# Kernel optimization log

Hardware: AMD Instinct MI355X
Metric: run time of the kernel (lower is better)

Reference implementation:

```python
import jax, jax.numpy as jnp
import numpy as np

N = 2048      # nodes (= in_features = out_features, forced by h0 @ adj)
C = 512       # channels
B = 8         # batch
NNZ = 65536   # number of edges (avg degree 32)
NEG = -9e15   # masked-fill value from the source


def setup_inputs() -> dict:
    key = jax.random.key(0)
    k1, k2, k3, k4 = jax.random.split(key, 4)
    x = jax.random.normal(k1, (B, C, N), dtype=jnp.float32)
    # xavier_normal_ with gain=0.01: std = gain * sqrt(2/(fan_in+fan_out))
    std = 0.01 * float(np.sqrt(2.0 / (N + N)))
    W1 = jax.random.normal(k2, (N, N), dtype=jnp.float32) * std
    W2 = jax.random.normal(k3, (N, N), dtype=jnp.float32) * std
    # e is initialized to 1 in the source; perturb so softmax is non-trivial
    e = 1.0 + 0.1 * jax.random.normal(k4, (NNZ,), dtype=jnp.float32)
    # flat row-major indices of mask nonzeros, unique + sorted (matches adj[mask] = e)
    rng = np.random.default_rng(0)
    edge_idx = np.sort(rng.choice(N * N, size=NNZ, replace=False)).astype(np.int64)
    return {"x": x, "W1": W1, "W2": W2, "e": e, "edge_idx": jnp.asarray(edge_idx)}


def reference(x, W1, W2, e, edge_idx):
    # h0, h1: [B, C, N]
    h0 = jnp.matmul(x, W1)
    h1 = jnp.matmul(x, W2)
    # scatter per-edge logits into dense [N, N], masked positions = -9e15
    logits = jnp.full((N * N,), NEG, dtype=jnp.float32).at[edge_idx].set(e)
    A = jax.nn.softmax(logits.reshape(N, N), axis=1)  # row-wise softmax
    diag = jnp.diagonal(A)                 # A * I  (self term, diagonal scaling)
    A_off = A - jnp.diag(diag)             # A * (1 - I)  (neighbor term)
    # h0 @ (A*I) == h0 scaled per-node by diag; h1 @ (A*(1-I)) dense GEMM
    out = h0 * diag[None, None, :] + jnp.matmul(h1, A_off)
    return out  # [B, C, N]; torch squeeze is a no-op here; bias=False
```

## Files before the change

### kernel.cpp

```cpp
#include <hip/hip_runtime.h>
#include <hip/hip_bf16.h>
#include <stdint.h>

#define NN 2048
#define LOG2NN 11
#define GK 2048
#define GNC 2048

typedef __bf16 bf16x8 __attribute__((ext_vector_type(8)));
typedef float f32x4 __attribute__((ext_vector_type(4)));

__device__ __forceinline__ ushort f2bf(float f) {
  uint32_t x = __float_as_uint(f);
  uint32_t r = (x + 0x7fffu + ((x >> 16) & 1u)) >> 16;
  return (ushort)r;
}

__global__ __launch_bounds__(256) void prep_kernel(
    const float* __restrict__ W1, const float* __restrict__ W2,
    ushort* __restrict__ WT, ushort* __restrict__ W2T,
    const float* __restrict__ x, ushort* __restrict__ xb,
    int* __restrict__ hist, float* __restrict__ uW, int* __restrict__ ecnt) {
  __shared__ float tile[64][65];
  const int bid = blockIdx.x;
  const int t = threadIdx.x;
  if (bid < 2048) {
    const int m = bid >> 10;
    const int rem = bid & 1023;
    const int r0 = (rem >> 5) * 64, c0 = (rem & 31) * 64;
    const float* in = m ? W2 : W1;
    ushort* out = m ? W2T : WT;
    const int tx = t & 15, ty = t >> 4;
#pragma unroll
    for (int i = 0; i < 4; ++i) {
      int r = i * 16 + ty;
      float4 v = *reinterpret_cast<const float4*>(&in[(size_t)(r0 + r) * NN + c0 + tx * 4]);
      tile[r][tx * 4 + 0] = v.x;
      tile[r][tx * 4 + 1] = v.y;
      tile[r][tx * 4 + 2] = v.z;
      tile[r][tx * 4 + 3] = v.w;
    }
    __syncthreads();
#pragma unroll
    for (int i = 0; i < 4; ++i) {
      int oc = i * 16 + ty;
      ushort4 o;
      o.x = f2bf(tile[tx * 4 + 0][oc]);
      o.y = f2bf(tile[tx * 4 + 1][oc]);
      o.z = f2bf(tile[tx * 4 + 2][oc]);
      o.w = f2bf(tile[tx * 4 + 3][oc]);
      *reinterpret_cast<ushort4*>(&out[(size_t)(c0 + oc) * NN + r0 + tx * 4]) = o;
    }
  } else if (bid < 6144) {
    int i = (bid - 2048) * 256 + t;
    const float4* in4 = reinterpret_cast<const float4*>(x);
    float4 a = in4[2 * i];
    float4 b = in4[2 * i + 1];
    uint4 o;
    o.x = (uint32_t)f2bf(a.x) | ((uint32_t)f2bf(a.y) << 16);
    o.y = (uint32_t)f2bf(a.z) | ((uint32_t)f2bf(a.w) << 16);
    o.z = (uint32_t)f2bf(b.x) | ((uint32_t)f2bf(b.y) << 16);
    o.w = (uint32_t)f2bf(b.z) | ((uint32_t)f2bf(b.w) << 16);
    reinterpret_cast<uint4*>(xb)[i] = o;
  } else {
#pragma unroll
    for (int j = 0; j < 8; ++j) {
      hist[t * 8 + j] = 0;
      uW[t * 8 + j] = 0.f;
    }
    if (t == 0) *ecnt = 0;
  }
}

__device__ __forceinline__ int lower_bound32(const int* __restrict__ a, int n, int v) {
  int lo = 0, hi = n;
  while (lo < hi) {
    int mid = (lo + hi) >> 1;
    if (a[mid] < v) lo = mid + 1; else hi = mid;
  }
  return lo;
}

__global__ __launch_bounds__(256) void softmax_hist_kernel(
    const int* __restrict__ idx, const float* __restrict__ e, int nnz,
    float* __restrict__ vals, float* __restrict__ diag, int* __restrict__ empty,
    int* __restrict__ ecnt, int* __restrict__ hist) {
  const int w = threadIdx.x >> 6, lane = threadIdx.x & 63;
  const int r = blockIdx.x * 4 + w;
  int lo = lower_bound32(idx, nnz, r << LOG2NN);
  int hi = lower_bound32(idx, nnz, (r + 1) << LOG2NN);
  if (hi <= lo) {
    if (lane == 0) { diag[r] = 1.0f / NN; empty[r] = 1; atomicAdd(ecnt, 1); }
    return;
  }
  float m = -3.0e38f;
  for (int j = lo + lane; j < hi; j += 64) m = fmaxf(m, e[j]);
#pragma unroll
  for (int s = 32; s >= 1; s >>= 1) m = fmaxf(m, __shfl_xor(m, s));
  float sum = 0.f;
  for (int j = lo + lane; j < hi; j += 64) sum += expf(e[j] - m);
#pragma unroll
  for (int s = 32; s >= 1; s >>= 1) sum += __shfl_xor(sum, s);
  float inv = 1.0f / sum;
  float dv = 0.f;
  for (int j = lo + lane; j < hi; j += 64) {
    float v = expf(e[j] - m) * inv;
    vals[j] = v;
    int c = idx[j] & (NN - 1);
    if (c == r) dv = v;
    else atomicAdd(&hist[c], 1);
  }
#pragma unroll
  for (int s = 32; s >= 1; s >>= 1) dv += __shfl_xor(dv, s);
  if (lane == 0) { diag[r] = dv; empty[r] = 0; }
}

__global__ __launch_bounds__(256) void scan_uw_kernel(
    const int* __restrict__ hist, int* __restrict__ base, int* __restrict__ cursor,
    const float* __restrict__ W2, const int* __restrict__ empty,
    const int* __restrict__ ecnt, float* __restrict__ uW) {
  if (blockIdx.x == 0) {
    const int l = threadIdx.x;
    if (l >= 64) return;
    int vals[32], pre[32];
    int run = 0;
#pragma unroll
    for (int j = 0; j < 32; ++j) {
      vals[j] = hist[l * 32 + j];
      pre[j] = run;
      run += vals[j];
    }
    int tot = run, inc = run;
#pragma unroll
    for (int s = 1; s < 64; s <<= 1) {
      int o = __shfl_up(inc, s);
      if (l >= s) inc += o;
    }
    int excl = inc - tot;
#pragma unroll
    for (int j = 0; j < 32; ++j) {
      int b = excl + pre[j];
      base[l * 32 + j] = b;
      cursor[l * 32 + j] = b;
    }
  } else {
    if (*ecnt == 0) return;
    int p = (blockIdx.x - 1) * 256 + threadIdx.x;
    float s = 0.f;
    for (int k = 0; k < NN; ++k)
      if (empty[k]) s += W2[(size_t)p * NN + k];
    uW[p] = s * (1.0f / NN);
  }
}

__global__ void scatter_kernel(const int* __restrict__ idx, const float* __restrict__ vals,
                               int nnz, int* __restrict__ cursor,
                               int* __restrict__ ek, float* __restrict__ ev) {
  int j = blockIdx.x * blockDim.x + threadIdx.x;
  if (j >= nnz) return;
  int f = idx[j];
  int c = f & (NN - 1), r = f >> LOG2NN;
  if (c != r) {
    int p = atomicAdd(&cursor[c], 1);
    ek[p] = r;
    ev[p] = vals[j];
  }
}

__global__ __launch_bounds__(256) void spmm_kernel(
    const int* __restrict__ ek, const float* __restrict__ ev,
    const int* __restrict__ base, const int* __restrict__ hist,
    const ushort* __restrict__ W2T,
    const float* __restrict__ diag, const int* __restrict__ empty,
    const float* __restrict__ uW, ushort* WT) {
  const int w = threadIdx.x >> 6, lane = threadIdx.x & 63;
  const int n = blockIdx.x * 2 + (w >> 1);
  const int c0 = (w & 1) * 1024 + lane * 16;
  const int start = base[n], cnt = hist[n];
  float acc[2][8];
#pragma unroll
  for (int g = 0; g < 2; ++g) {
    float4 u0 = *reinterpret_cast<const float4*>(&uW[c0 + g * 8]);
    float4 u1 = *reinterpret_cast<const float4*>(&uW[c0 + g * 8 + 4]);
    acc[g][0] = u0.x; acc[g][1] = u0.y; acc[g][2] = u0.z; acc[g][3] = u0.w;
    acc[g][4] = u1.x; acc[g][5] = u1.y; acc[g][6] = u1.z; acc[g][7] = u1.w;
  }
  float d = diag[n];
  if (d != 0.f) {
#pragma unroll
    for (int g = 0; g < 2; ++g) {
      bf16x8 wd = *reinterpret_cast<const bf16x8*>(&WT[(size_t)n * NN + c0 + g * 8]);
#pragma unroll
      for (int j = 0; j < 8; ++j) acc[g][j] += d * (float)wd[j];
    }
  }
  int i = 0;
  for (; i + 4 <= cnt; i += 4) {
    int k[4];
    float v[4];
    bf16x8 wv[4][2];
#pragma unroll
    for (int e2 = 0; e2 < 4; ++e2) {
      k[e2] = ek[start + i + e2];
      v[e2] = ev[start + i + e2];
    }
#pragma unroll
    for (int e2 = 0; e2 < 4; ++e2)
#pragma unroll
      for (int g = 0; g < 2; ++g)
        wv[e2][g] = *reinterpret_cast<const bf16x8*>(&W2T[(size_t)k[e2] * NN + c0 + g * 8]);
#pragma unroll
    for (int e2 = 0; e2 < 4; ++e2)
#pragma unroll
      for (int g = 0; g < 2; ++g)
#pragma unroll
        for (int j = 0; j < 8; ++j)
          acc[g][j] += v[e2] * (float)wv[e2][g][j];
  }
  for (; i < cnt; ++i) {
    int k0 = ek[start + i];
    float v0 = ev[start + i];
#pragma unroll
    for (int g = 0; g < 2; ++g) {
      bf16x8 w0 = *reinterpret_cast<const bf16x8*>(&W2T[(size_t)k0 * NN + c0 + g * 8]);
#pragma unroll
      for (int j = 0; j < 8; ++j) acc[g][j] += v0 * (float)w0[j];
    }
  }
  if (empty[n]) {
#pragma unroll
    for (int g = 0; g < 2; ++g) {
      bf16x8 we = *reinterpret_cast<const bf16x8*>(&W2T[(size_t)n * NN + c0 + g * 8]);
#pragma unroll
      for (int j = 0; j < 8; ++j) acc[g][j] -= (1.0f / NN) * (float)we[j];
    }
  }
#pragma unroll
  for (int g = 0; g < 2; ++g) {
    uint4 o;
    o.x = (uint32_t)f2bf(acc[g][0]) | ((uint32_t)f2bf(acc[g][1]) << 16);
    o.y = (uint32_t)f2bf(acc[g][2]) | ((uint32_t)f2bf(acc[g][3]) << 16);
    o.z = (uint32_t)f2bf(acc[g][4]) | ((uint32_t)f2bf(acc[g][5]) << 16);
    o.w = (uint32_t)f2bf(acc[g][6]) | ((uint32_t)f2bf(acc[g][7]) << 16);
    *reinterpret_cast<uint4*>(&WT[(size_t)n * NN + c0 + g * 8]) = o;
  }
}

__device__ __forceinline__ void gload_lds16(const ushort* g, char* l) {
  __builtin_amdgcn_global_load_lds(
      (__attribute__((address_space(1))) uint32_t*)(uintptr_t)g,
      (__attribute__((address_space(3))) uint32_t*)l, 16, 0, 0);
}

__global__ __launch_bounds__(256)
void gemm_bt_kernel(const ushort* __restrict__ A, const ushort* __restrict__ Bt,
                    float* __restrict__ Cf) {
  __shared__ ushort As[128 * 32];
  __shared__ ushort Bs[128 * 32];
  const int t = threadIdx.x;
  const int wid = t >> 6;
  const int lane = t & 63;
  const int m0 = blockIdx.y * 128;
  const int n0 = blockIdx.x * 128;
  const int wm = wid >> 1, wn = wid & 1;

  f32x4 acc[4][4] = {};

  const ushort* Ag0 = A + (size_t)(m0 + (t >> 2)) * GK + (t & 3) * 8;
  const ushort* Ag1 = Ag0 + (size_t)64 * GK;
  const ushort* Bg0 = Bt + (size_t)(n0 + (t >> 2)) * GK + (t & 3) * 8;
  const ushort* Bg1 = Bg0 + (size_t)64 * GK;
  char* AsW = (char*)As + wid * 1024;
  char* BsW = (char*)Bs + wid * 1024;

  const int fr = lane & 15, fg = lane >> 4;
  const ushort* ArdA = As + (size_t)(wm * 64 + fr) * 32 + fg * 8;
  const ushort* ArdB = Bs + (size_t)(wn * 64 + fr) * 32 + fg * 8;

  for (int kt = 0; kt < GK; kt += 32) {
    gload_lds16(Ag0 + kt, AsW);
    gload_lds16(Ag1 + kt, AsW + 4096);
    gload_lds16(Bg0 + kt, BsW);
    gload_lds16(Bg1 + kt, BsW + 4096);
    __syncthreads();
    bf16x8 af[4], bb[4];
#pragma unroll
    for (int i = 0; i < 4; ++i) af[i] = *reinterpret_cast<const bf16x8*>(ArdA + i * 16 * 32);
#pragma unroll
    for (int i = 0; i < 4; ++i) bb[i] = *reinterpret_cast<const bf16x8*>(ArdB + i * 16 * 32);
#pragma unroll
    for (int i = 0; i < 4; ++i)
#pragma unroll
      for (int j = 0; j < 4; ++j)
        acc[i][j] = __builtin_amdgcn_mfma_f32_16x16x32_bf16(af[i], bb[j], acc[i][j], 0, 0, 0);
    __syncthreads();
  }

  const int cr = lane >> 4, cc = lane & 15;
#pragma unroll
  for (int i = 0; i < 4; ++i)
#pragma unroll
    for (int j = 0; j < 4; ++j)
#pragma unroll
      for (int q = 0; q < 4; ++q) {
        int grow = m0 + wm * 64 + i * 16 + cr * 4 + q;
        int gcol = n0 + wn * 64 + j * 16 + cc;
        Cf[(size_t)grow * GNC + gcol] = acc[i][j][q];
      }
}

extern "C" void kernel_launch(void* const* d_in, const int* in_sizes, int n_in,
                              void* d_out, int out_size, void* d_ws, size_t ws_size,
                              hipStream_t stream) {
  const float* x   = (const float*)d_in[0];
  const float* W1  = (const float*)d_in[1];
  const float* W2  = (const float*)d_in[2];
  const float* e   = (const float*)d_in[3];
  const int*   eix = (const int*)d_in[4];
  const int nnz = in_sizes[3];
  float* out = (float*)d_out;

  char* w = (char*)d_ws;
  ushort* W2T  = (ushort*)w; w += (size_t)NN * NN * 2;
  ushort* WT   = (ushort*)w; w += (size_t)NN * NN * 2;
  ushort* xb   = (ushort*)w; w += (size_t)4096 * NN * 2;
  float*  vals = (float*)w;  w += (size_t)nnz * 4;
  int*    ek   = (int*)w;    w += (size_t)nnz * 4;
  float*  ev   = (float*)w;  w += (size_t)nnz * 4;
  int*    hist = (int*)w;    w += NN * 4;
  int*    base = (int*)w;    w += NN * 4;
  int*    curs = (int*)w;    w += NN * 4;
  float*  diag = (float*)w;  w += NN * 4;
  int*    empt = (int*)w;    w += NN * 4;
  float*  uW   = (float*)w;  w += NN * 4;
  int*    ecnt = (int*)w;    w += 256;

  prep_kernel<<<dim3(6145), dim3(256), 0, stream>>>(W1, W2, WT, W2T, x, xb,
                                                    hist, uW, ecnt);
  softmax_hist_kernel<<<dim3(512), dim3(256), 0, stream>>>(eix, e, nnz, vals,
                                                           diag, empt, ecnt, hist);
  scan_uw_kernel<<<dim3(9), dim3(256), 0, stream>>>(hist, base, curs, W2, empt,
                                                    ecnt, uW);
  scatter_kernel<<<dim3((nnz + 255) / 256), dim3(256), 0, stream>>>(eix, vals, nnz,
                                                                    curs, ek, ev);
  spmm_kernel<<<dim3(1024), dim3(256), 0, stream>>>(ek, ev, base, hist, W2T,
                                                    diag, empt, uW, WT);
  gemm_bt_kernel<<<dim3(16, 32), dim3(256), 0, stream>>>(xb, WT, out);
}
```

Measured before the change: 125.0 us.

## Rewrite final GEMM as 256x256 tile, 8-wave, double-buffered ping-pong kernel

Replaces the simple 128x128 single-buffer bf16 MFMA GEMM with a 256x256-tile, 512-thread kernel. It uses a 64-wide K step, a double-buffered 128KB LDS with XOR swizzling, and a grid swizzle over blocks. Global-to-LDS loads for later K tiles are interleaved with four MFMA quadrant phases, using setprio, sched barriers and partial vmcnt waits to overlap memory with compute. This is meant to remove the exposed load latency and low arithmetic intensity of the old kernel. In exchange it launches only 128 blocks, which may underfill the CUs, and the hand-tuned wait counts are fragile.

```diff
diff --git a/kernel.cpp b/kernel.cpp
--- a/kernel.cpp
+++ b/kernel.cpp
@@ -252,61 +252,127 @@
       (__attribute__((address_space(3))) uint32_t*)l, 16, 0, 0);
 }
 
-__global__ __launch_bounds__(256)
-void gemm_bt_kernel(const ushort* __restrict__ A, const ushort* __restrict__ Bt,
-                    float* __restrict__ Cf) {
-  __shared__ ushort As[128 * 32];
-  __shared__ ushort Bs[128 * 32];
+#define NT 32
+
+__global__ __launch_bounds__(512, 2)
+void gemm8_kernel(const ushort* __restrict__ A, const ushort* __restrict__ Bt,
+                  float* __restrict__ Cf) {
+  __shared__ __align__(16) char smem[131072];
   const int t = threadIdx.x;
-  const int wid = t >> 6;
-  const int lane = t & 63;
-  const int m0 = blockIdx.y * 128;
-  const int n0 = blockIdx.x * 128;
-  const int wm = wid >> 1, wn = wid & 1;
-
-  f32x4 acc[4][4] = {};
-
-  const ushort* Ag0 = A + (size_t)(m0 + (t >> 2)) * GK + (t & 3) * 8;
-  const ushort* Ag1 = Ag0 + (size_t)64 * GK;
-  const ushort* Bg0 = Bt + (size_t)(n0 + (t >> 2)) * GK + (t & 3) * 8;
-  const ushort* Bg1 = Bg0 + (size_t)64 * GK;
-  char* AsW = (char*)As + wid * 1024;
-  char* BsW = (char*)Bs + wid * 1024;
-
+  const int wid = t >> 6, lane = t & 63;
+  const int wm = wid >> 2, wn = wid & 3;
   const int fr = lane & 15, fg = lane >> 4;
-  const ushort* ArdA = As + (size_t)(wm * 64 + fr) * 32 + fg * 8;
-  const ushort* ArdB = Bs + (size_t)(wn * 64 + fr) * 32 + fg * 8;
-
-  for (int kt = 0; kt < GK; kt += 32) {
-    gload_lds16(Ag0 + kt, AsW);
-    gload_lds16(Ag1 + kt, AsW + 4096);
-    gload_lds16(Bg0 + kt, BsW);
-    gload_lds16(Bg1 + kt, BsW + 4096);
-    __syncthreads();
-    bf16x8 af[4], bb[4];
-#pragma unroll
-    for (int i = 0; i < 4; ++i) af[i] = *reinterpret_cast<const bf16x8*>(ArdA + i * 16 * 32);
-#pragma unroll
-    for (int i = 0; i < 4; ++i) bb[i] = *reinterpret_cast<const bf16x8*>(ArdB + i * 16 * 32);
-#pragma unroll
-    for (int i = 0; i < 4; ++i)
-#pragma unroll
-      for (int j = 0; j < 4; ++j)
-        acc[i][j] = __builtin_amdgcn_mfma_f32_16x16x32_bf16(af[i], bb[j], acc[i][j], 0, 0, 0);
-    __syncthreads();
-  }
-
+
+  const int swz = ((int)blockIdx.x & 7) * 16 + ((int)blockIdx.x >> 3);
+  const int m0 = (swz >> 3) * 256;
+  const int n0 = (swz & 7) * 256;
+
+  const int l8 = lane >> 3;
+  const int scol = ((lane & 7) ^ l8) << 3;
+  const int srow = wid * 8 + l8;
+
+#define STG(PTR, BASE0, MATOFF, H, TAU) do {                                   \
+    const int _b = (TAU) & 1;                                                  \
+    gload_lds16((PTR) + (size_t)((BASE0) + (H) * 128 + srow) * GK +            \
+                    (TAU) * 64 + scol,                                         \
+                smem + (MATOFF) + _b * 32768 + (H) * 16384 + wid * 1024);      \
+    gload_lds16((PTR) + (size_t)((BASE0) + (H) * 128 + 64 + srow) * GK +       \
+                    (TAU) * 64 + scol,                                         \
+                smem + (MATOFF) + _b * 32768 + (H) * 16384 + 8192 + wid * 1024); \
+  } while (0)
+
+  const int sw = (fr & 7) << 4;
+  const int ko0 = (fg * 16) ^ sw;
+  const int ko1 = (64 + fg * 16) ^ sw;
+  const int arow = (wm * 16 + fr) * 128;
+  const int brow = (wn * 32 + fr) * 128;
+
+  f32x4 acc[2][2][4][2] = {};
+  bf16x8 aF[4][2], b0F[2][2], b1F[2][2];
+
+#define LDA(MQ, B_) do {                                                       \
+    _Pragma("unroll") for (int mf = 0; mf < 4; ++mf) {                         \
+      const char* _p = smem + (B_) * 32768 + arow + ((MQ) * 128 + mf * 32) * 128; \
+      aF[mf][0] = *reinterpret_cast<const bf16x8*>(_p + ko0);                  \
+      aF[mf][1] = *reinterpret_cast<const bf16x8*>(_p + ko1);                  \
+    }                                                                          \
+  } while (0)
+
+#define LDB(DST, NQ, B_) do {                                                  \
+    _Pragma("unroll") for (int nf = 0; nf < 2; ++nf) {                         \
+      const char* _p = smem + 65536 + (B_) * 32768 + brow +                    \
+                       ((NQ) * 128 + nf * 16) * 128;                           \
+      DST[nf][0] = *reinterpret_cast<const bf16x8*>(_p + ko0);                 \
+      DST[nf][1] = *reinterpret_cast<const bf16x8*>(_p + ko1);                 \
+    }                                                                          \
+  } while (0)
+
+#define MM(MQ, NQ, BF) do {                                                    \
+    _Pragma("unroll") for (int mf = 0; mf < 4; ++mf)                           \
+      _Pragma("unroll") for (int nf = 0; nf < 2; ++nf) {                       \
+        acc[MQ][NQ][mf][nf] = __builtin_amdgcn_mfma_f32_16x16x32_bf16(         \
+            aF[mf][0], BF[nf][0], acc[MQ][NQ][mf][nf], 0, 0, 0);               \
+        acc[MQ][NQ][mf][nf] = __builtin_amdgcn_mfma_f32_16x16x32_bf16(         \
+            aF[mf][1], BF[nf][1], acc[MQ][NQ][mf][nf], 0, 0, 0);               \
+      }                                                                        \
+  } while (0)
+
+#define PHASE_MID() do {                                                       \
+    __builtin_amdgcn_s_barrier();                                              \
+    asm volatile("s_waitcnt lgkmcnt(0)" ::: "memory");                         \
+    __builtin_amdgcn_sched_barrier(0);                                         \
+    __builtin_amdgcn_s_setprio(1);                                             \
+  } while (0)
+
+#define PHASE_END() do {                                                       \
+    __builtin_amdgcn_s_setprio(0);                                             \
+    __builtin_amdgcn_s_barrier();                                              \
+  } while (0)
+
+  STG(A, m0, 0, 0, 0);      STG(Bt, n0, 65536, 0, 0);
+  STG(A, m0, 0, 1, 0);      STG(Bt, n0, 65536, 1, 0);
+  STG(A, m0, 0, 0, 1);      STG(Bt, n0, 65536, 0, 1);
+  STG(A, m0, 0, 1, 1);
+  asm volatile("s_waitcnt vmcnt(6)" ::: "memory");
+  __builtin_amdgcn_sched_barrier(0);
+  __builtin_amdgcn_s_barrier();
+
+  for (int kt = 0; kt < NT; ++kt) {
+    const int b = kt & 1;
+    const int t1 = (kt + 1) & (NT - 1), t2 = (kt + 2) & (NT - 1);
+    LDA(0, b); LDB(b0F, 0, b);
+    STG(Bt, n0, 65536, 1, t1);
+    PHASE_MID(); MM(0, 0, b0F); PHASE_END();
+    LDB(b1F, 1, b);
+    STG(A, m0, 0, 0, t2);
+    PHASE_MID(); MM(0, 1, b1F); PHASE_END();
+    LDA(1, b);
+    STG(Bt, n0, 65536, 0, t2);
+    PHASE_MID(); MM(1, 0, b0F); PHASE_END();
+    STG(A, m0, 0, 1, t2);
+    PHASE_MID(); MM(1, 1, b1F);
+    __builtin_amdgcn_s_setprio(0);
+    asm volatile("s_waitcnt vmcnt(6)" ::: "memory");
+    __builtin_amdgcn_sched_barrier(0);
+    __builtin_amdgcn_s_barrier();
+  }
+
+  asm volatile("s_waitcnt vmcnt(0)" ::: "memory");
   const int cr = lane >> 4, cc = lane & 15;
 #pragma unroll
-  for (int i = 0; i < 4; ++i)
-#pragma unroll
-    for (int j = 0; j < 4; ++j)
-#pragma unroll
-      for (int q = 0; q < 4; ++q) {
-        int grow = m0 + wm * 64 + i * 16 + cr * 4 + q;
-        int gcol = n0 + wn * 64 + j * 16 + cc;
-        Cf[(size_t)grow * GNC + gcol] = acc[i][j][q];
-      }
+  for (int mq = 0; mq < 2; ++mq)
+#pragma unroll
+    for (int nq = 0; nq < 2; ++nq)
+#pragma unroll
+      for (int mf = 0; mf < 4; ++mf)
+#pragma unroll
+        for (int nf = 0; nf < 2; ++nf)
+#pragma unroll
+          for (int q = 0; q < 4; ++q) {
+            int gm = m0 + mq * 128 + mf * 32 + wm * 16 + cr * 4 + q;
+            int gn = n0 + nq * 128 + wn * 32 + nf * 16 + cc;
+            Cf[(size_t)gm * GNC + gn] = acc[mq][nq][mf][nf][q];
+          }
 }
 
 extern "C" void kernel_launch(void* const* d_in, const int* in_sizes, int n_in,
@@ -345,5 +411,5 @@
                                                                     curs, ek, ev);
   spmm_kernel<<<dim3(1024), dim3(256), 0, stream>>>(ek, ev, base, hist, W2T,
                                                     diag, empt, uW, WT);
-  gemm_bt_kernel<<<dim3(16, 32), dim3(256), 0, stream>>>(xb, WT, out);
-}
+  gemm8_kernel<<<dim3(128), dim3(512), 0, stream>>>(xb, WT, out);
+}
```

Result: no change. 125.5 us (+0.4%).
